# Kernel optimization log

Hardware: AMD Instinct MI355X
Metric: run time of the kernel (lower is better)

Reference implementation:

```python
import jax, jax.numpy as jnp
import numpy as np

V, E, S, B, N, H = 32000, 1024, 1024, 4, 4, 16
DH = E // H
DFF = 4 * E
EPS = 1e-6


def _sinusoidal_pe(max_len, d):
    pos = np.arange(max_len)[:, None].astype(np.float32)
    div = np.power(10000.0, np.arange(0, d, 2).astype(np.float32) / d)
    pe = np.zeros((max_len, d), dtype=np.float32)
    pe[:, 0::2] = np.sin(pos / div)
    pe[:, 1::2] = np.cos(pos / div)
    return jnp.asarray(pe)


def layer_norm(x, g, b):
    mu = jnp.mean(x, axis=-1, keepdims=True)
    var = jnp.var(x, axis=-1, keepdims=True)
    return (x - mu) * jax.lax.rsqrt(var + EPS) * g + b


def setup_inputs() -> dict:
    key = jax.random.key(0)
    ks = iter(jax.random.split(key, 32))
    s = 0.02
    d = {}
    d['tokens'] = jax.random.randint(next(ks), (B, S), 0, V)
    d['emb'] = jax.random.normal(next(ks), (V, E), jnp.float32) * s
    d['pe'] = _sinusoidal_pe(S, E)
    # stacked per-layer params, leading dim N
    for name, shape in [('Wq', (N, E, E)), ('Wk', (N, E, E)), ('Wv', (N, E, E)), ('Wo', (N, E, E)),
                        ('W1', (N, E, DFF)), ('W2', (N, DFF, E))]:
        d[name] = jax.random.normal(next(ks), shape, jnp.float32) * s
    for name, shape in [('bq', (N, E)), ('bk', (N, E)), ('bv', (N, E)), ('bo', (N, E)),
                        ('b1', (N, DFF)), ('b2', (N, E))]:
        d[name] = jnp.zeros(shape, jnp.float32)
    d['ln1_g'] = jnp.ones((N, E)); d['ln1_b'] = jnp.zeros((N, E))
    d['ln2_g'] = jnp.ones((N, E)); d['ln2_b'] = jnp.zeros((N, E))
    d['enc_g'] = jnp.ones((E,)); d['enc_b'] = jnp.zeros((E,))
    d['fin_g'] = jnp.ones((E,)); d['fin_b'] = jnp.zeros((E,))
    d['Wout'] = jax.random.normal(next(ks), (E, V), jnp.float32) * s
    d['bout'] = jnp.zeros((V,), jnp.float32)
    return d


def _mha(x, Wq, bq, Wk, bk, Wv, bv, Wo, bo):
    b, s, _ = x.shape
    q = (x @ Wq + bq).reshape(b, s, H, DH)
    k = (x @ Wk + bk).reshape(b, s, H, DH)
    v = (x @ Wv + bv).reshape(b, s, H, DH)
    scores = jnp.einsum('bqhd,bkhd->bhqk', q, k) / jnp.sqrt(jnp.float32(DH))
    attn = jax.nn.softmax(scores, axis=-1)
    out = jnp.einsum('bhqk,bkhd->bqhd', attn, v).reshape(b, s, E)
    return out @ Wo + bo


def reference(tokens, emb, pe, Wq, bq, Wk, bk, Wv, bv, Wo, bo,
              W1, b1, W2, b2, ln1_g, ln1_b, ln2_g, ln2_b,
              enc_g, enc_b, fin_g, fin_b, Wout, bout):
    x = emb[tokens] + pe[None, :tokens.shape[1]]  # [B,S,E]; dropout = identity (eval)
    for i in range(N):
        # sublayer 0: x + LN(MHA(x))  (source's unusual residual order)
        a = _mha(x, Wq[i], bq[i], Wk[i], bk[i], Wv[i], bv[i], Wo[i], bo[i])
        x = x + layer_norm(a, ln1_g[i], ln1_b[i])
        # sublayer 1: x + LN(FF(x))
        f = jax.nn.relu(x @ W1[i] + b1[i]) @ W2[i] + b2[i]
        x = x + layer_norm(f, ln2_g[i], ln2_b[i])
    x = layer_norm(x, enc_g, enc_b)      # encoder final LN
    x = layer_norm(x, fin_g, fin_b)      # Transformer-level LN
    return x @ Wout + bout               # [B,S,V]
```

## Files before the change

### kernel.cpp

```cpp
#include <hip/hip_runtime.h>
#include <hip/hip_bf16.h>
#include <stdint.h>

#define EDIM 1024
#define DFFDIM 4096
#define NLAYER 4
#define BATCH 4
#define SEQ 1024
#define NHEAD 16
#define DHEAD 64
#define VOCAB 32000
#define MROWS (BATCH*SEQ)
#define QKVLD (3*EDIM)
#define EPSF 1e-6f
#define ALPHA 0.18033688011112043f

typedef float f32x4 __attribute__((ext_vector_type(4)));
typedef short s16x8 __attribute__((ext_vector_type(8)));
typedef __bf16 bf16x8 __attribute__((ext_vector_type(8)));

__device__ inline unsigned short f2bf(float f) {
  union { float f; uint32_t u; } v; v.f = f;
  uint32_t r = v.u + 0x7fffu + ((v.u >> 16) & 1u);
  return (unsigned short)(r >> 16);
}

__device__ __forceinline__ float fexp2(float x) {
  float r; asm("v_exp_f32 %0, %1" : "=v"(r) : "v"(x)); return r;
}
__device__ __forceinline__ uint32_t cvtpk(float lo, float hi) {
  uint32_t r; asm("v_cvt_pk_bf16_f32 %0, %1, %2" : "=v"(r) : "v"(lo), "v"(hi)); return r;
}

__device__ __forceinline__ void gload16(const void* g, void* l) {
  __builtin_amdgcn_global_load_lds(
      (const __attribute__((address_space(1))) void*)g,
      (__attribute__((address_space(3))) void*)l, 16, 0, 0);
}

__global__ __launch_bounds__(256) void embed_kernel(
    const int* __restrict__ tokens, const float* __restrict__ emb,
    const float* __restrict__ pe, float* __restrict__ x,
    unsigned short* __restrict__ xb) {
  const int row = blockIdx.x;
  const int s = row & (SEQ - 1);
  const int tok = tokens[row];
  const int c = threadIdx.x * 4;
  float4 ev = *(const float4*)(emb + (size_t)tok * EDIM + c);
  float4 pv = *(const float4*)(pe + (size_t)s * EDIM + c);
  float4 o;
  o.x = ev.x + pv.x; o.y = ev.y + pv.y; o.z = ev.z + pv.z; o.w = ev.w + pv.w;
  *(float4*)(x + (size_t)row * EDIM + c) = o;
  unsigned short* xr = xb + (size_t)row * EDIM + c;
  xr[0] = f2bf(o.x); xr[1] = f2bf(o.y); xr[2] = f2bf(o.z); xr[3] = f2bf(o.w);
}

__global__ __launch_bounds__(256) void transpose_w(
    const float* __restrict__ src0, unsigned short* __restrict__ dst0,
    int N, int K, float scale, size_t srcStride, size_t dstStride) {
  const float* src = src0 + (size_t)blockIdx.z * srcStride;
  unsigned short* dst = dst0 + (size_t)blockIdx.z * dstStride;
  __shared__ float tl[64][65];
  const int t = threadIdx.x;
  const int k0 = blockIdx.x * 64, n0 = blockIdx.y * 64;
  const int c = (t & 15) * 4, r0 = t >> 4;
  #pragma unroll
  for (int i = 0; i < 4; ++i) {
    const int r = r0 + i * 16;
    float4 v = *(const float4*)(src + (size_t)(k0 + r) * N + n0 + c);
    tl[r][c] = v.x; tl[r][c + 1] = v.y; tl[r][c + 2] = v.z; tl[r][c + 3] = v.w;
  }
  __syncthreads();
  #pragma unroll
  for (int i = 0; i < 4; ++i) {
    const int n = r0 + i * 16;
    uint2 o;
    o.x = (uint32_t)f2bf(tl[c + 0][n] * scale) | ((uint32_t)f2bf(tl[c + 1][n] * scale) << 16);
    o.y = (uint32_t)f2bf(tl[c + 2][n] * scale) | ((uint32_t)f2bf(tl[c + 3][n] * scale) << 16);
    *(uint2*)(dst + (size_t)(n0 + n) * K + k0 + c) = o;
  }
}

__global__ __launch_bounds__(256) void pack_bias(
    const float* __restrict__ bq, const float* __restrict__ bk,
    const float* __restrict__ bv, float* __restrict__ dst) {
  const int idx = blockIdx.x * 256 + threadIdx.x;
  if (idx >= NLAYER * QKVLD) return;
  const int layer = idx / QKVLD, c = idx % QKVLD;
  float v;
  if (c < 1024)      v = bq[layer * 1024 + c] * ALPHA;
  else if (c < 2048) v = bk[layer * 1024 + c - 1024];
  else               v = bv[layer * 1024 + c - 2048];
  dst[idx] = v;
}

template<int BM, int OUT_BF16, int RELU, int SPLITK>
__global__ __launch_bounds__(BM * 2, (BM == 256) ? 2 : 3) void gemm3(
    const unsigned short* __restrict__ A, const unsigned short* __restrict__ Bt,
    const float* __restrict__ bias, void* __restrict__ Cout, void* __restrict__ C2,
    int Nld, int KLEN, int KLD, int NBLK, int G) {
  constexpr int BUFB = BM * 128;
  constexpr int ABYTES = BM * 64;
  constexpr int WN = (BM == 256) ? 4 : 2;
  constexpr int MF = BM / 32;
  __shared__ __attribute__((aligned(16))) char smb[3 * BUFB];
  const int t = threadIdx.x, lane = t & 63;
  const int wave = t >> 6;
  const int wr = wave / WN, wc = wave % WN;
  const int l15 = lane & 15, lg = lane >> 4;

  const int cpx = gridDim.x >> 3;
  const int bid = blockIdx.x;
  const int swz = (bid & 7) * cpx + (bid >> 3);
  const int sg = (gridDim.x / NBLK) * G;
  const int ns = swz / sg, rem = swz % sg;
  const int m0 = (rem / G) * BM;
  const int n0 = (ns * G + rem % G) * BM;
  const int koff = SPLITK ? blockIdx.y * KLEN : 0;

  f32x4 acc[MF][4];
  #pragma unroll
  for (int i = 0; i < MF; ++i)
    #pragma unroll
    for (int j = 0; j < 4; ++j)
      acc[i][j] = (f32x4){0.f, 0.f, 0.f, 0.f};

  const int srow = t >> 2;
  const int scol = (((t & 3) ^ ((t >> 3) & 3)) << 3);
  const unsigned short* agp = A  + (size_t)(m0 + srow) * KLD + scol + koff;
  const unsigned short* bgp = Bt + (size_t)(n0 + srow) * KLD + scol + koff;
  const size_t rhalf = (size_t)(BM / 2) * KLD;

  const int cxo = (lg * 16) ^ (((l15 >> 1) & 3) << 4);
  const int rdA = (wr * (BM / 2) + l15) * 64 + cxo;
  const int rdB = ABYTES + (wc * 64 + l15) * 64 + cxo;

  auto stage_tile = [&](int b, int kt) {
    const int k0 = kt * 32;
    char* d = smb + b * BUFB + t * 16;
    gload16(agp + k0, d);
    gload16(agp + rhalf + k0, d + BM * 32);
    gload16(bgp + k0, d + ABYTES);
    gload16(bgp + rhalf + k0, d + ABYTES + BM * 32);
  };

  const int NT = KLEN / 32;
  stage_tile(0, 0);
  stage_tile(1, 1);
  asm volatile("s_waitcnt vmcnt(4)" ::: "memory");
  __builtin_amdgcn_s_barrier();
  __builtin_amdgcn_sched_barrier(0);

  int bufc = 0, bufn = 2;
  for (int tt = 0; tt < NT; ++tt) {
    if (tt + 2 < NT) stage_tile(bufn, tt + 2);

    const char* ab = smb + bufc * BUFB;
    bf16x8 af[MF], bf[4];
    #pragma unroll
    for (int mf = 0; mf < MF; ++mf)
      af[mf] = *(const bf16x8*)(ab + rdA + mf * 1024);
    #pragma unroll
    for (int nf = 0; nf < 4; ++nf)
      bf[nf] = *(const bf16x8*)(ab + rdB + nf * 1024);

    __builtin_amdgcn_s_setprio(1);
    #pragma unroll
    for (int mf = 0; mf < MF; ++mf)
      #pragma unroll
      for (int nf = 0; nf < 4; ++nf)
        acc[mf][nf] = __builtin_amdgcn_mfma_f32_16x16x32_bf16(af[mf], bf[nf], acc[mf][nf], 0, 0, 0);
    __builtin_amdgcn_s_setprio(0);

    if (tt + 2 < NT)      asm volatile("s_waitcnt vmcnt(4)" ::: "memory");
    else if (tt + 1 < NT) asm volatile("s_waitcnt vmcnt(0)" ::: "memory");
    __builtin_amdgcn_sched_barrier(0);
    __builtin_amdgcn_s_barrier();
    __builtin_amdgcn_sched_barrier(0);

    bufc = (bufc == 2) ? 0 : bufc + 1;
    bufn = (bufn == 2) ? 0 : bufn + 1;
  }

  void* Cw = (SPLITK && blockIdx.y) ? C2 : Cout;
  #pragma unroll
  for (int mf = 0; mf < MF; ++mf) {
    #pragma unroll
    for (int nf = 0; nf < 4; ++nf) {
      const int col = n0 + wc * 64 + nf * 16 + l15;
      const float bv = (SPLITK && blockIdx.y) ? 0.f : bias[col];
      #pragma unroll
      for (int r = 0; r < 4; ++r) {
        const int row = m0 + wr * (BM / 2) + mf * 16 + lg * 4 + r;
        float val = acc[mf][nf][r] + bv;
        if (RELU) val = fmaxf(val, 0.f);
        if (OUT_BF16)
          ((unsigned short*)Cw)[(size_t)row * Nld + col] = f2bf(val);
        else
          ((float*)Cw)[(size_t)row * Nld + col] = val;
      }
    }
  }
}

__global__ __launch_bounds__(256) void attn_kernel(
    const unsigned short* __restrict__ qkv, unsigned short* __restrict__ ctx) {
  const int b = blockIdx.z, h = blockIdx.y;
  const int t = threadIdx.x, wave = t >> 6, lane = t & 63;
  const int l15 = lane & 15, lg = lane >> 4;
  const int qrow0 = blockIdx.x * 64 + wave * 16;
  const unsigned short* qbs = qkv + (size_t)b * SEQ * QKVLD + h * DHEAD;
  const unsigned short* kbs = qbs + EDIM;
  const unsigned short* vbs = qbs + 2 * EDIM;
  __shared__ unsigned short Ksm[64][72];
  __shared__ unsigned short VTs[64 * 64];

  const unsigned short* qp = qbs + (size_t)(qrow0 + l15) * QKVLD + lg * 8;
  bf16x8 a0 = *(const bf16x8*)qp;
  bf16x8 a1 = *(const bf16x8*)(qp + 32);

  f32x4 o[4];
  #pragma unroll
  for (int dg = 0; dg < 4; ++dg) o[dg] = (f32x4){0.f, 0.f, 0.f, 0.f};
  float m = -1e30f, ls = 0.f;

  const int sr = t >> 2;
  const int sc = (t & 3) * 16;
  const int posw = (((sr >> 4) & 1) << 5) | (((sr & 15) >> 2) << 3) | (((sr >> 5) & 1) << 2) | (sr & 3);
  const unsigned short* kgp = kbs + (size_t)sr * QKVLD + sc;
  const unsigned short* vgp = vbs + (size_t)sr * QKVLD + sc;
  const size_t tilestep = (size_t)64 * QKVLD;

  s16x8 kr0 = *(const s16x8*)kgp, kr1 = *(const s16x8*)(kgp + 8);
  s16x8 vr0 = *(const s16x8*)vgp, vr1 = *(const s16x8*)(vgp + 8);

  const int NT = SEQ / 64;
  for (int j = 0; j < NT; ++j) {
    *(s16x8*)&Ksm[sr][sc] = kr0;
    *(s16x8*)&Ksm[sr][sc + 8] = kr1;
    #pragma unroll
    for (int c = 0; c < 2; ++c) {
      s16x8 vv = c ? vr1 : vr0;
      #pragma unroll
      for (int e = 0; e < 8; ++e) {
        const int d = sc + c * 8 + e;
        const int byteo = d * 128 + ((posw * 2) ^ ((d & 7) << 4));
        *(unsigned short*)((char*)VTs + byteo) = (unsigned short)vv[e];
      }
    }
    __syncthreads();

    f32x4 s[4];
    __builtin_amdgcn_s_setprio(1);
    #pragma unroll
    for (int g = 0; g < 4; ++g) {
      bf16x8 k0 = *(const bf16x8*)&Ksm[g * 16 + l15][lg * 8];
      bf16x8 k1 = *(const bf16x8*)&Ksm[g * 16 + l15][32 + lg * 8];
      f32x4 z = {0, 0, 0, 0};
      z = __builtin_amdgcn_mfma_f32_16x16x32_bf16(k0, a0, z, 0, 0, 0);
      s[g] = __builtin_amdgcn_mfma_f32_16x16x32_bf16(k1, a1, z, 0, 0, 0);
    }
    __builtin_amdgcn_s_setprio(0);

    if (j + 1 < NT) {
      const unsigned short* kn = kgp + (size_t)(j + 1) * tilestep;
      const unsigned short* vn = vgp + (size_t)(j + 1) * tilestep;
      kr0 = *(const s16x8*)kn; kr1 = *(const s16x8*)(kn + 8);
      vr0 = *(const s16x8*)vn; vr1 = *(const s16x8*)(vn + 8);
    }

    float mx = s[0][0];
    #pragma unroll
    for (int g = 0; g < 4; ++g)
      #pragma unroll
      for (int r = 0; r < 4; ++r) mx = fmaxf(mx, s[g][r]);
    mx = fmaxf(mx, __shfl_xor(mx, 16));
    mx = fmaxf(mx, __shfl_xor(mx, 32));

    if (__any(mx > m + 8.f)) {
      const float mn = fmaxf(m, mx);
      const float scl = fexp2(m - mn);
      m = mn;
      ls *= scl;
      #pragma unroll
      for (int dg = 0; dg < 4; ++dg)
        #pragma unroll
        for (int r = 0; r < 4; ++r) o[dg][r] *= scl;
    }
    #pragma unroll
    for (int g = 0; g < 4; ++g)
      #pragma unroll
      for (int r = 0; r < 4; ++r) s[g][r] = fexp2(s[g][r] - m);

    float rs = 0.f;
    #pragma unroll
    for (int g = 0; g < 4; ++g)
      rs += (s[g][0] + s[g][1]) + (s[g][2] + s[g][3]);
    rs += __shfl_xor(rs, 16);
    rs += __shfl_xor(rs, 32);
    ls += rs;

    union { uint32_t u[4]; bf16x8 v; } pb0, pb1;
    pb0.u[0] = cvtpk(s[0][0], s[0][1]); pb0.u[1] = cvtpk(s[0][2], s[0][3]);
    pb0.u[2] = cvtpk(s[2][0], s[2][1]); pb0.u[3] = cvtpk(s[2][2], s[2][3]);
    pb1.u[0] = cvtpk(s[1][0], s[1][1]); pb1.u[1] = cvtpk(s[1][2], s[1][3]);
    pb1.u[2] = cvtpk(s[3][0], s[3][1]); pb1.u[3] = cvtpk(s[3][2], s[3][3]);

    auto vld = [&](int dg, int c) {
      const int byteo = (dg * 16 + l15) * 128 + ((c * 64 + lg * 16) ^ ((l15 & 7) << 4));
      return *(const bf16x8*)((const char*)VTs + byteo);
    };
    __builtin_amdgcn_s_setprio(1);
    #pragma unroll
    for (int dg = 0; dg < 4; ++dg)
      o[dg] = __builtin_amdgcn_mfma_f32_16x16x32_bf16(vld(dg, 0), pb0.v, o[dg], 0, 0, 0);
    #pragma unroll
    for (int dg = 0; dg < 4; ++dg)
      o[dg] = __builtin_amdgcn_mfma_f32_16x16x32_bf16(vld(dg, 1), pb1.v, o[dg], 0, 0, 0);
    __builtin_amdgcn_s_setprio(0);
    __syncthreads();
  }

  unsigned short* cp = ctx + (size_t)b * SEQ * EDIM + h * DHEAD + (size_t)(qrow0 + l15) * EDIM;
  const float inv = 1.f / ls;
  #pragma unroll
  for (int dg = 0; dg < 4; ++dg) {
    uint2 w;
    w.x = cvtpk(o[dg][0] * inv, o[dg][1] * inv);
    w.y = cvtpk(o[dg][2] * inv, o[dg][3] * inv);
    *(uint2*)(cp + dg * 16 + lg * 4) = w;
  }
}

template<int TWO>
__global__ __launch_bounds__(256) void ln_add_kernel(
    const float* __restrict__ a, const float* __restrict__ a2,
    const float* __restrict__ g, const float* __restrict__ bb,
    float* __restrict__ x, unsigned short* __restrict__ xb) {
  const int row = blockIdx.x, t = threadIdx.x;
  float4 av = *(const float4*)(a + (size_t)row * EDIM + t * 4);
  if (TWO) {
    float4 a2v = *(const float4*)(a2 + (size_t)row * EDIM + t * 4);
    av.x += a2v.x; av.y += a2v.y; av.z += a2v.z; av.w += a2v.w;
  }
  float s = av.x + av.y + av.z + av.w;
  float qq = av.x * av.x + av.y * av.y + av.z * av.z + av.w * av.w;
  #pragma unroll
  for (int off = 1; off < 64; off <<= 1) { s += __shfl_xor(s, off); qq += __shfl_xor(qq, off); }
  __shared__ float red[8];
  const int wv = t >> 6;
  if ((t & 63) == 0) { red[wv] = s; red[4 + wv] = qq; }
  __syncthreads();
  s = red[0] + red[1] + red[2] + red[3];
  qq = red[4] + red[5] + red[6] + red[7];
  const float mean = s * (1.f / EDIM);
  const float rstd = rsqrtf(qq * (1.f / EDIM) - mean * mean + EPSF);
  float4 gv = *(const float4*)(g + t * 4);
  float4 bv = *(const float4*)(bb + t * 4);
  float* xr = x + (size_t)row * EDIM;
  float4 xv = *(float4*)(xr + t * 4);
  float4 o;
  o.x = xv.x + (av.x - mean) * rstd * gv.x + bv.x;
  o.y = xv.y + (av.y - mean) * rstd * gv.y + bv.y;
  o.z = xv.z + (av.z - mean) * rstd * gv.z + bv.z;
  o.w = xv.w + (av.w - mean) * rstd * gv.w + bv.w;
  *(float4*)(xr + t * 4) = o;
  unsigned short* xbr = xb + (size_t)row * EDIM + t * 4;
  xbr[0] = f2bf(o.x); xbr[1] = f2bf(o.y); xbr[2] = f2bf(o.z); xbr[3] = f2bf(o.w);
}

__global__ __launch_bounds__(256) void final_ln_kernel(
    const float* __restrict__ x, const float* __restrict__ g1, const float* __restrict__ b1,
    const float* __restrict__ g2, const float* __restrict__ b2,
    unsigned short* __restrict__ xb) {
  const int row = blockIdx.x, t = threadIdx.x;
  __shared__ float red[8];
  const int wv = t >> 6;
  const float* xr = x + (size_t)row * EDIM;
  float4 v = *(const float4*)(xr + t * 4);

  float s = v.x + v.y + v.z + v.w;
  float qq = v.x * v.x + v.y * v.y + v.z * v.z + v.w * v.w;
  #pragma unroll
  for (int off = 1; off < 64; off <<= 1) { s += __shfl_xor(s, off); qq += __shfl_xor(qq, off); }
  if ((t & 63) == 0) { red[wv] = s; red[4 + wv] = qq; }
  __syncthreads();
  s = red[0] + red[1] + red[2] + red[3];
  qq = red[4] + red[5] + red[6] + red[7];
  __syncthreads();
  float mean = s * (1.f / EDIM);
  float rstd = rsqrtf(qq * (1.f / EDIM) - mean * mean + EPSF);
  float4 g1v = *(const float4*)(g1 + t * 4);
  float4 b1v = *(const float4*)(b1 + t * 4);
  float4 tv;
  tv.x = (v.x - mean) * rstd * g1v.x + b1v.x;
  tv.y = (v.y - mean) * rstd * g1v.y + b1v.y;
  tv.z = (v.z - mean) * rstd * g1v.z + b1v.z;
  tv.w = (v.w - mean) * rstd * g1v.w + b1v.w;

  s = tv.x + tv.y + tv.z + tv.w;
  qq = tv.x * tv.x + tv.y * tv.y + tv.z * tv.z + tv.w * tv.w;
  #pragma unroll
  for (int off = 1; off < 64; off <<= 1) { s += __shfl_xor(s, off); qq += __shfl_xor(qq, off); }
  if ((t & 63) == 0) { red[wv] = s; red[4 + wv] = qq; }
  __syncthreads();
  s = red[0] + red[1] + red[2] + red[3];
  qq = red[4] + red[5] + red[6] + red[7];
  mean = s * (1.f / EDIM);
  rstd = rsqrtf(qq * (1.f / EDIM) - mean * mean + EPSF);
  float4 g2v = *(const float4*)(g2 + t * 4);
  float4 b2v = *(const float4*)(b2 + t * 4);
  unsigned short* o = xb + (size_t)row * EDIM + t * 4;
  o[0] = f2bf((tv.x - mean) * rstd * g2v.x + b2v.x);
  o[1] = f2bf((tv.y - mean) * rstd * g2v.y + b2v.y);
  o[2] = f2bf((tv.z - mean) * rstd * g2v.z + b2v.z);
  o[3] = f2bf((tv.w - mean) * rstd * g2v.w + b2v.w);
}

extern "C" void kernel_launch(void* const* d_in, const int* in_sizes, int n_in,
                              void* d_out, int out_size, void* d_ws, size_t ws_size,
                              hipStream_t stream) {
  const int*   tokens = (const int*)d_in[0];
  const float* emb    = (const float*)d_in[1];
  const float* pe     = (const float*)d_in[2];
  const float* Wq     = (const float*)d_in[3];
  const float* Wk     = (const float*)d_in[4];
  const float* Wv     = (const float*)d_in[5];
  const float* Wo     = (const float*)d_in[6];
  const float* W1     = (const float*)d_in[7];
  const float* W2     = (const float*)d_in[8];
  const float* bq     = (const float*)d_in[9];
  const float* bk     = (const float*)d_in[10];
  const float* bv     = (const float*)d_in[11];
  const float* bo     = (const float*)d_in[12];
  const float* b1     = (const float*)d_in[13];
  const float* b2     = (const float*)d_in[14];
  const float* ln1_g  = (const float*)d_in[15];
  const float* ln1_b  = (const float*)d_in[16];
  const float* ln2_g  = (const float*)d_in[17];
  const float* ln2_b  = (const float*)d_in[18];
  const float* enc_g  = (const float*)d_in[19];
  const float* enc_b  = (const float*)d_in[20];
  const float* fin_g  = (const float*)d_in[21];
  const float* fin_b  = (const float*)d_in[22];
  const float* Wout   = (const float*)d_in[23];
  const float* bout   = (const float*)d_in[24];
  float* out = (float*)d_out;

  uint8_t* p = (uint8_t*)d_ws;
  auto alloc = [&](size_t bytes) {
    void* r = (void*)p;
    p += (bytes + 255) & ~(size_t)255;
    return r;
  };
  float*          x     = (float*)alloc((size_t)MROWS * EDIM * 4);
  unsigned short* xb    = (unsigned short*)alloc((size_t)MROWS * EDIM * 2);
  float*          tbuf  = (float*)alloc((size_t)MROWS * EDIM * 4);
  unsigned short* qkv   = (unsigned short*)alloc((size_t)MROWS * QKVLD * 2);
  unsigned short* ctx   = (unsigned short*)alloc((size_t)MROWS * EDIM * 2);
  unsigned short* wlt   = (unsigned short*)alloc((size_t)NLAYER * 12 * 1024 * 1024 * 2);
  unsigned short* woutt = (unsigned short*)alloc((size_t)VOCAB * EDIM * 2);
  float*          bqkv  = (float*)alloc((size_t)NLAYER * QKVLD * 4);
  unsigned short* ff1   = qkv;
  if ((size_t)(p - (uint8_t*)d_ws) > ws_size) return;
  float* tbuf2 = (float*)alloc((size_t)MROWS * EDIM * 4);
  const bool have2 = (size_t)(p - (uint8_t*)d_ws) <= ws_size;

  const dim3 blk(256);
  const dim3 blk512(512);
  const size_t LW = (size_t)12 * 1024 * 1024;
  const size_t M1 = 1024 * 1024;

  transpose_w<<<dim3(16, 16, NLAYER), blk, 0, stream>>>(Wq, wlt,          1024, 1024, ALPHA, M1, LW);
  transpose_w<<<dim3(16, 16, NLAYER), blk, 0, stream>>>(Wk, wlt + M1,     1024, 1024, 1.0f,  M1, LW);
  transpose_w<<<dim3(16, 16, NLAYER), blk, 0, stream>>>(Wv, wlt + 2 * M1, 1024, 1024, 1.0f,  M1, LW);
  transpose_w<<<dim3(16, 16, NLAYER), blk, 0, stream>>>(Wo, wlt + 3 * M1, 1024, 1024, 1.0f,  M1, LW);
  transpose_w<<<dim3(16, 64, NLAYER), blk, 0, stream>>>(W1, wlt + 4 * M1, 4096, 1024, 1.0f, 4 * M1, LW);
  transpose_w<<<dim3(64, 16, NLAYER), blk, 0, stream>>>(W2, wlt + 8 * M1, 1024, 4096, 1.0f, 4 * M1, LW);
  transpose_w<<<dim3(16, 500), blk, 0, stream>>>(Wout, woutt, VOCAB, 1024, 1.0f, 0, 0);
  pack_bias<<<(NLAYER * QKVLD + 255) / 256, blk, 0, stream>>>(bq, bk, bv, bqkv);

  embed_kernel<<<MROWS, blk, 0, stream>>>(tokens, emb, pe, x, xb);

  const int MB2 = MROWS / 256;
  const int MB1 = MROWS / 128;
  for (int i = 0; i < NLAYER; ++i) {
    unsigned short* lb = wlt + (size_t)i * LW;
    gemm3<128, 1, 0, 0><<<MB1 * (QKVLD / 128), blk, 0, stream>>>(
        xb, lb, bqkv + (size_t)i * QKVLD, qkv, nullptr, QKVLD, EDIM, EDIM, QKVLD / 128, 8);
    attn_kernel<<<dim3(SEQ / 64, NHEAD, BATCH), blk, 0, stream>>>(qkv, ctx);
    if (have2) {
      gemm3<128, 0, 0, 1><<<dim3(MB1 * (EDIM / 128), 2), blk, 0, stream>>>(
          ctx, lb + 3 * M1, bo + i * EDIM, tbuf, tbuf2, EDIM, EDIM / 2, EDIM, EDIM / 128, 8);
      ln_add_kernel<1><<<MROWS, blk, 0, stream>>>(tbuf, tbuf2, ln1_g + i * EDIM, ln1_b + i * EDIM, x, xb);
    } else {
      gemm3<128, 0, 0, 0><<<MB1 * (EDIM / 128), blk, 0, stream>>>(
          ctx, lb + 3 * M1, bo + i * EDIM, tbuf, nullptr, EDIM, EDIM, EDIM, EDIM / 128, 8);
      ln_add_kernel<0><<<MROWS, blk, 0, stream>>>(tbuf, nullptr, ln1_g + i * EDIM, ln1_b + i * EDIM, x, xb);
    }
    gemm3<128, 1, 1, 0><<<MB1 * (DFFDIM / 128), blk, 0, stream>>>(
        xb, lb + 4 * M1, b1 + i * DFFDIM, ff1, nullptr, DFFDIM, EDIM, EDIM, DFFDIM / 128, 8);
    if (have2) {
      gemm3<128, 0, 0, 1><<<dim3(MB1 * (EDIM / 128), 2), blk, 0, stream>>>(
          ff1, lb + 8 * M1, b2 + i * EDIM, tbuf, tbuf2, EDIM, DFFDIM / 2, DFFDIM, EDIM / 128, 8);
      ln_add_kernel<1><<<MROWS, blk, 0, stream>>>(tbuf, tbuf2, ln2_g + i * EDIM, ln2_b + i * EDIM, x, xb);
    } else {
      gemm3<128, 0, 0, 0><<<MB1 * (EDIM / 128), blk, 0, stream>>>(
          ff1, lb + 8 * M1, b2 + i * EDIM, tbuf, nullptr, EDIM, DFFDIM, DFFDIM, EDIM / 128, 8);
      ln_add_kernel<0><<<MROWS, blk, 0, stream>>>(tbuf, nullptr, ln2_g + i * EDIM, ln2_b + i * EDIM, x, xb);
    }
  }

  final_ln_kernel<<<MROWS, blk, 0, stream>>>(x, enc_g, enc_b, fin_g, fin_b, xb);
  gemm3<256, 0, 0, 0><<<MB2 * (VOCAB / 256), blk512, 0, stream>>>(
      xb, woutt, bout, out, nullptr, VOCAB, EDIM, EDIM, VOCAB / 256, 5);
}
```

Measured before the change: 1.318 ms.

## Process two 16-row query tiles per wave in attention kernel

After: 1.292 ms. 2.0% less time.

```diff
diff --git a/kernel.cpp b/kernel.cpp
--- a/kernel.cpp
+++ b/kernel.cpp
@@ -208,21 +208,24 @@
   const int b = blockIdx.z, h = blockIdx.y;
   const int t = threadIdx.x, wave = t >> 6, lane = t & 63;
   const int l15 = lane & 15, lg = lane >> 4;
-  const int qrow0 = blockIdx.x * 64 + wave * 16;
+  const int qBase = blockIdx.x * 128 + wave * 32;
   const unsigned short* qbs = qkv + (size_t)b * SEQ * QKVLD + h * DHEAD;
   const unsigned short* kbs = qbs + EDIM;
   const unsigned short* vbs = qbs + 2 * EDIM;
   __shared__ unsigned short Ksm[64][72];
   __shared__ unsigned short VTs[64 * 64];
 
-  const unsigned short* qp = qbs + (size_t)(qrow0 + l15) * QKVLD + lg * 8;
-  bf16x8 a0 = *(const bf16x8*)qp;
-  bf16x8 a1 = *(const bf16x8*)(qp + 32);
-
-  f32x4 o[4];
-  #pragma unroll
-  for (int dg = 0; dg < 4; ++dg) o[dg] = (f32x4){0.f, 0.f, 0.f, 0.f};
-  float m = -1e30f, ls = 0.f;
+  const unsigned short* qpA = qbs + (size_t)(qBase + l15) * QKVLD + lg * 8;
+  const unsigned short* qpB = qbs + (size_t)(qBase + 16 + l15) * QKVLD + lg * 8;
+  bf16x8 aA0 = *(const bf16x8*)qpA;
+  bf16x8 aA1 = *(const bf16x8*)(qpA + 32);
+  bf16x8 aB0 = *(const bf16x8*)qpB;
+  bf16x8 aB1 = *(const bf16x8*)(qpB + 32);
+
+  f32x4 oA[4], oB[4];
+  #pragma unroll
+  for (int dg = 0; dg < 4; ++dg) { oA[dg] = (f32x4){0,0,0,0}; oB[dg] = (f32x4){0,0,0,0}; }
+  float mA = -1e30f, lsA = 0.f, mB = -1e30f, lsB = 0.f;
 
   const int sr = t >> 2;
   const int sc = (t & 3) * 16;
@@ -250,15 +253,17 @@
     }
     __syncthreads();
 
-    f32x4 s[4];
+    f32x4 sA[4], sB[4];
     __builtin_amdgcn_s_setprio(1);
     #pragma unroll
     for (int g = 0; g < 4; ++g) {
       bf16x8 k0 = *(const bf16x8*)&Ksm[g * 16 + l15][lg * 8];
       bf16x8 k1 = *(const bf16x8*)&Ksm[g * 16 + l15][32 + lg * 8];
-      f32x4 z = {0, 0, 0, 0};
-      z = __builtin_amdgcn_mfma_f32_16x16x32_bf16(k0, a0, z, 0, 0, 0);
-      s[g] = __builtin_amdgcn_mfma_f32_16x16x32_bf16(k1, a1, z, 0, 0, 0);
+      f32x4 zA = {0,0,0,0}, zB = {0,0,0,0};
+      zA = __builtin_amdgcn_mfma_f32_16x16x32_bf16(k0, aA0, zA, 0, 0, 0);
+      sA[g] = __builtin_amdgcn_mfma_f32_16x16x32_bf16(k1, aA1, zA, 0, 0, 0);
+      zB = __builtin_amdgcn_mfma_f32_16x16x32_bf16(k0, aB0, zB, 0, 0, 0);
+      sB[g] = __builtin_amdgcn_mfma_f32_16x16x32_bf16(k1, aB1, zB, 0, 0, 0);
     }
     __builtin_amdgcn_s_setprio(0);
 
@@ -269,42 +274,48 @@
       vr0 = *(const s16x8*)vn; vr1 = *(const s16x8*)(vn + 8);
     }
 
-    float mx = s[0][0];
+    float mxA = sA[0][0], mxB = sB[0][0];
     #pragma unroll
     for (int g = 0; g < 4; ++g)
       #pragma unroll
-      for (int r = 0; r < 4; ++r) mx = fmaxf(mx, s[g][r]);
-    mx = fmaxf(mx, __shfl_xor(mx, 16));
-    mx = fmaxf(mx, __shfl_xor(mx, 32));
-
-    if (__any(mx > m + 8.f)) {
-      const float mn = fmaxf(m, mx);
-      const float scl = fexp2(m - mn);
-      m = mn;
-      ls *= scl;
+      for (int r = 0; r < 4; ++r) { mxA = fmaxf(mxA, sA[g][r]); mxB = fmaxf(mxB, sB[g][r]); }
+    mxA = fmaxf(mxA, __shfl_xor(mxA, 16)); mxA = fmaxf(mxA, __shfl_xor(mxA, 32));
+    mxB = fmaxf(mxB, __shfl_xor(mxB, 16)); mxB = fmaxf(mxB, __shfl_xor(mxB, 32));
+
+    if (__any((mxA > mA + 8.f) || (mxB > mB + 8.f))) {
+      const float mnA = fmaxf(mA, mxA), mnB = fmaxf(mB, mxB);
+      const float sclA = fexp2(mA - mnA), sclB = fexp2(mB - mnB);
+      mA = mnA; mB = mnB;
+      lsA *= sclA; lsB *= sclB;
       #pragma unroll
       for (int dg = 0; dg < 4; ++dg)
         #pragma unroll
-        for (int r = 0; r < 4; ++r) o[dg][r] *= scl;
+        for (int r = 0; r < 4; ++r) { oA[dg][r] *= sclA; oB[dg][r] *= sclB; }
     }
     #pragma unroll
     for (int g = 0; g < 4; ++g)
       #pragma unroll
-      for (int r = 0; r < 4; ++r) s[g][r] = fexp2(s[g][r] - m);
-
-    float rs = 0.f;
-    #pragma unroll
-    for (int g = 0; g < 4; ++g)
-      rs += (s[g][0] + s[g][1]) + (s[g][2] + s[g][3]);
-    rs += __shfl_xor(rs, 16);
-    rs += __shfl_xor(rs, 32);
-    ls += rs;
-
-    union { uint32_t u[4]; bf16x8 v; } pb0, pb1;
-    pb0.u[0] = cvtpk(s[0][0], s[0][1]); pb0.u[1] = cvtpk(s[0][2], s[0][3]);
-    pb0.u[2] = cvtpk(s[2][0], s[2][1]); pb0.u[3] = cvtpk(s[2][2], s[2][3]);
-    pb1.u[0] = cvtpk(s[1][0], s[1][1]); pb1.u[1] = cvtpk(s[1][2], s[1][3]);
-    pb1.u[2] = cvtpk(s[3][0], s[3][1]); pb1.u[3] = cvtpk(s[3][2], s[3][3]);
+      for (int r = 0; r < 4; ++r) { sA[g][r] = fexp2(sA[g][r] - mA); sB[g][r] = fexp2(sB[g][r] - mB); }
+
+    float rsA = 0.f, rsB = 0.f;
+    #pragma unroll
+    for (int g = 0; g < 4; ++g) {
+      rsA += (sA[g][0] + sA[g][1]) + (sA[g][2] + sA[g][3]);
+      rsB += (sB[g][0] + sB[g][1]) + (sB[g][2] + sB[g][3]);
+    }
+    rsA += __shfl_xor(rsA, 16); rsA += __shfl_xor(rsA, 32);
+    rsB += __shfl_xor(rsB, 16); rsB += __shfl_xor(rsB, 32);
+    lsA += rsA; lsB += rsB;
+
+    union { uint32_t u[4]; bf16x8 v; } pA0, pA1, pB0, pB1;
+    pA0.u[0] = cvtpk(sA[0][0], sA[0][1]); pA0.u[1] = cvtpk(sA[0][2], sA[0][3]);
+    pA0.u[2] = cvtpk(sA[2][0], sA[2][1]); pA0.u[3] = cvtpk(sA[2][2], sA[2][3]);
+    pA1.u[0] = cvtpk(sA[1][0], sA[1][1]); pA1.u[1] = cvtpk(sA[1][2], sA[1][3]);
+    pA1.u[2] = cvtpk(sA[3][0], sA[3][1]); pA1.u[3] = cvtpk(sA[3][2], sA[3][3]);
+    pB0.u[0] = cvtpk(sB[0][0], sB[0][1]); pB0.u[1] = cvtpk(sB[0][2], sB[0][3]);
+    pB0.u[2] = cvtpk(sB[2][0], sB[2][1]); pB0.u[3] = cvtpk(sB[2][2], sB[2][3]);
+    pB1.u[0] = cvtpk(sB[1][0], sB[1][1]); pB1.u[1] = cvtpk(sB[1][2], sB[1][3]);
+    pB1.u[2] = cvtpk(sB[3][0], sB[3][1]); pB1.u[3] = cvtpk(sB[3][2], sB[3][3]);
 
     auto vld = [&](int dg, int c) {
       const int byteo = (dg * 16 + l15) * 128 + ((c * 64 + lg * 16) ^ ((l15 & 7) << 4));
@@ -312,23 +323,34 @@
     };
     __builtin_amdgcn_s_setprio(1);
     #pragma unroll
-    for (int dg = 0; dg < 4; ++dg)
-      o[dg] = __builtin_amdgcn_mfma_f32_16x16x32_bf16(vld(dg, 0), pb0.v, o[dg], 0, 0, 0);
-    #pragma unroll
-    for (int dg = 0; dg < 4; ++dg)
-      o[dg] = __builtin_amdgcn_mfma_f32_16x16x32_bf16(vld(dg, 1), pb1.v, o[dg], 0, 0, 0);
+    for (int dg = 0; dg < 4; ++dg) {
+      bf16x8 v0 = vld(dg, 0);
+      oA[dg] = __builtin_amdgcn_mfma_f32_16x16x32_bf16(v0, pA0.v, oA[dg], 0, 0, 0);
+      oB[dg] = __builtin_amdgcn_mfma_f32_16x16x32_bf16(v0, pB0.v, oB[dg], 0, 0, 0);
+    }
+    #pragma unroll
+    for (int dg = 0; dg < 4; ++dg) {
+      bf16x8 v1 = vld(dg, 1);
+      oA[dg] = __builtin_amdgcn_mfma_f32_16x16x32_bf16(v1, pA1.v, oA[dg], 0, 0, 0);
+      oB[dg] = __builtin_amdgcn_mfma_f32_16x16x32_bf16(v1, pB1.v, oB[dg], 0, 0, 0);
+    }
     __builtin_amdgcn_s_setprio(0);
     __syncthreads();
   }
 
-  unsigned short* cp = ctx + (size_t)b * SEQ * EDIM + h * DHEAD + (size_t)(qrow0 + l15) * EDIM;
-  const float inv = 1.f / ls;
+  unsigned short* base = ctx + (size_t)b * SEQ * EDIM + h * DHEAD;
+  unsigned short* cpA = base + (size_t)(qBase + l15) * EDIM;
+  unsigned short* cpB = base + (size_t)(qBase + 16 + l15) * EDIM;
+  const float invA = 1.f / lsA, invB = 1.f / lsB;
   #pragma unroll
   for (int dg = 0; dg < 4; ++dg) {
-    uint2 w;
-    w.x = cvtpk(o[dg][0] * inv, o[dg][1] * inv);
-    w.y = cvtpk(o[dg][2] * inv, o[dg][3] * inv);
-    *(uint2*)(cp + dg * 16 + lg * 4) = w;
+    uint2 wA, wB;
+    wA.x = cvtpk(oA[dg][0] * invA, oA[dg][1] * invA);
+    wA.y = cvtpk(oA[dg][2] * invA, oA[dg][3] * invA);
+    wB.x = cvtpk(oB[dg][0] * invB, oB[dg][1] * invB);
+    wB.y = cvtpk(oB[dg][2] * invB, oB[dg][3] * invB);
+    *(uint2*)(cpA + dg * 16 + lg * 4) = wA;
+    *(uint2*)(cpB + dg * 16 + lg * 4) = wB;
   }
 }
 
@@ -488,7 +510,7 @@
     unsigned short* lb = wlt + (size_t)i * LW;
     gemm3<128, 1, 0, 0><<<MB1 * (QKVLD / 128), blk, 0, stream>>>(
         xb, lb, bqkv + (size_t)i * QKVLD, qkv, nullptr, QKVLD, EDIM, EDIM, QKVLD / 128, 8);
-    attn_kernel<<<dim3(SEQ / 64, NHEAD, BATCH), blk, 0, stream>>>(qkv, ctx);
+    attn_kernel<<<dim3(SEQ / 128, NHEAD, BATCH), blk, 0, stream>>>(qkv, ctx);
     if (have2) {
       gemm3<128, 0, 0, 1><<<dim3(MB1 * (EDIM / 128), 2), blk, 0, stream>>>(
           ctx, lb + 3 * M1, bo + i * EDIM, tbuf, tbuf2, EDIM, EDIM / 2, EDIM, EDIM / 128, 8);
```
